# Performance work log

Measured on AMD Instinct MI355X. Metric: run time of the kernel, lower is better.

Reference implementation:

```python
import jax, jax.numpy as jnp
import numpy as np
from functools import partial
from jax import lax

THRESHOLD = 1.0
BETA = 4.0

@partial(jax.custom_vjp, nondiff_argnums=(1, 2))
def spike_fn(membrane, threshold, beta):
    # hard threshold forward
    return (membrane >= threshold).astype(membrane.dtype)

def _spike_fwd(membrane, threshold, beta):
    return spike_fn(membrane, threshold, beta), membrane

def _spike_bwd(threshold, beta, membrane, g):
    # fast-sigmoid surrogate gradient: 1 / (1 + beta*|u - theta|)^2
    x = membrane - threshold
    surrogate = 1.0 / (1.0 + beta * jnp.abs(x)) ** 2
    return (g * surrogate,)

spike_fn.defvjp(_spike_fwd, _spike_bwd)


def setup_inputs() -> dict:
    key = jax.random.key(0)
    k1, = jax.random.split(key, 1)
    x = jax.random.normal(k1, (64, 100, 4096), dtype=jnp.float32)
    # log_alpha = log(exp(-1/tau_mem)) = -1/tau_mem, tau_mem = 20.0
    log_alpha = jnp.asarray(-1.0 / 20.0, dtype=jnp.float32)
    return {"x": x, "log_alpha": log_alpha}


def reference(x, log_alpha):
    # x: (batch, time, features)
    alpha = jax.nn.sigmoid(log_alpha)  # membrane decay in (0,1)

    def step(u, xt):
        u = alpha * u + xt                    # leaky integration
        s = spike_fn(u, THRESHOLD, BETA)      # fire
        u = u - s * THRESHOLD                 # subtract-reset
        return u, s

    x_t = jnp.swapaxes(x, 0, 1)               # (T, B, F)
    u0 = jnp.zeros_like(x_t[0])
    _, spikes_t = lax.scan(step, u0, x_t)
    spikes = jnp.swapaxes(spikes_t, 0, 1)      # (B, T, F)
    rate = spikes.mean()
    return spikes, rate
```

## Files before the change

### kernel.cpp

```cpp
#include <hip/hip_runtime.h>
#include <math.h>


typedef float f32x2 __attribute__((ext_vector_type(2)));

constexpr int T_STEPS = 100;
constexpr int F2      = 2048;
constexpr int BATCH   = 64;
constexpr long long TOTAL = (long long)BATCH * T_STEPS * 4096;

__global__ __launch_bounds__(256)
void lif_fwd(const f32x2* __restrict__ x,
             const float* __restrict__ log_alpha,
             f32x2*       __restrict__ out,
             unsigned int* __restrict__ cnt) {
    int idx  = blockIdx.x * 256 + threadIdx.x;
    int b    = idx >> 11;
    int f2   = idx & 2047;
    size_t base = (size_t)b * T_STEPS * F2 + f2;

    double la = (double)log_alpha[0];
    float alpha = (float)(1.0 / (1.0 + exp(-la)));

    f32x2 u = {0.f, 0.f};
    unsigned int c = 0;

    #pragma unroll 10
    for (int t = 0; t < T_STEPS; ++t) {
        f32x2 xt = x[base + (size_t)t * F2];
        f32x2 s;
        float ux = __fadd_rn(__fmul_rn(alpha, u.x), xt.x);
        float uy = __fadd_rn(__fmul_rn(alpha, u.y), xt.y);
        s.x = (ux >= 1.0f) ? 1.0f : 0.0f;
        s.y = (uy >= 1.0f) ? 1.0f : 0.0f;
        u.x = ux - s.x;
        u.y = uy - s.y;
        __builtin_nontemporal_store(s, &out[base + (size_t)t * F2]);
        c += (unsigned)(s.x + s.y);
    }

    for (int off = 32; off > 0; off >>= 1)
        c += __shfl_down(c, off, 64);

    __shared__ unsigned int wsum[4];
    int lane = threadIdx.x & 63;
    int wid  = threadIdx.x >> 6;
    if (lane == 0) wsum[wid] = c;
    __syncthreads();
    if (threadIdx.x == 0) {
        unsigned int s = wsum[0] + wsum[1] + wsum[2] + wsum[3];
        atomicAdd(cnt, s);
    }
}

__global__ void lif_rate(const unsigned int* __restrict__ cnt,
                         float* __restrict__ rate_out) {
    rate_out[0] = (float)((double)cnt[0] / (double)TOTAL);
}

extern "C" void kernel_launch(void* const* d_in, const int* in_sizes, int n_in,
                              void* d_out, int out_size, void* d_ws, size_t ws_size,
                              hipStream_t stream) {
    const float* x  = (const float*)d_in[0];
    const float* la = (const float*)d_in[1];
    float* out = (float*)d_out;
    unsigned int* cnt = (unsigned int*)d_ws;

    (void)hipMemsetAsync(cnt, 0, sizeof(unsigned int), stream);

    int threads = BATCH * F2;
    lif_fwd<<<threads / 256, 256, 0, stream>>>(
        (const f32x2*)x, la, (f32x2*)out, cnt);

    lif_rate<<<1, 1, 0, stream>>>(cnt, out + TOTAL);
}
```

Baseline: 43.20 us.

## Use one feature per thread and replace atomic counter with per-block partial sums

Result: faster. 37.73 us, median of 2 (-12.7%).

```diff
diff --git a/kernel.cpp b/kernel.cpp
--- a/kernel.cpp
+++ b/kernel.cpp
@@ -2,41 +2,36 @@
 #include <math.h>
 
 
-typedef float f32x2 __attribute__((ext_vector_type(2)));
-
 constexpr int T_STEPS = 100;
-constexpr int F2      = 2048;
+constexpr int F       = 4096;
 constexpr int BATCH   = 64;
-constexpr long long TOTAL = (long long)BATCH * T_STEPS * 4096;
+constexpr int NBLOCKS = BATCH * F / 256;
+constexpr long long TOTAL = (long long)BATCH * T_STEPS * F;
 
 __global__ __launch_bounds__(256)
-void lif_fwd(const f32x2* __restrict__ x,
+void lif_fwd(const float* __restrict__ x,
              const float* __restrict__ log_alpha,
-             f32x2*       __restrict__ out,
-             unsigned int* __restrict__ cnt) {
+             float*       __restrict__ out,
+             unsigned int* __restrict__ blk_cnt) {
     int idx  = blockIdx.x * 256 + threadIdx.x;
-    int b    = idx >> 11;
-    int f2   = idx & 2047;
-    size_t base = (size_t)b * T_STEPS * F2 + f2;
+    int b    = idx >> 12;
+    int f    = idx & 4095;
+    size_t base = (size_t)b * T_STEPS * F + f;
 
     double la = (double)log_alpha[0];
     float alpha = (float)(1.0 / (1.0 + exp(-la)));
 
-    f32x2 u = {0.f, 0.f};
+    float u = 0.f;
     unsigned int c = 0;
 
     #pragma unroll 10
     for (int t = 0; t < T_STEPS; ++t) {
-        f32x2 xt = x[base + (size_t)t * F2];
-        f32x2 s;
-        float ux = __fadd_rn(__fmul_rn(alpha, u.x), xt.x);
-        float uy = __fadd_rn(__fmul_rn(alpha, u.y), xt.y);
-        s.x = (ux >= 1.0f) ? 1.0f : 0.0f;
-        s.y = (uy >= 1.0f) ? 1.0f : 0.0f;
-        u.x = ux - s.x;
-        u.y = uy - s.y;
-        __builtin_nontemporal_store(s, &out[base + (size_t)t * F2]);
-        c += (unsigned)(s.x + s.y);
+        float xt = x[base + (size_t)t * F];
+        u = __fadd_rn(__fmul_rn(alpha, u), xt);
+        float s = (u >= 1.0f) ? 1.0f : 0.0f;
+        u -= s;
+        __builtin_nontemporal_store(s, &out[base + (size_t)t * F]);
+        c += (unsigned)s;
     }
 
     for (int off = 32; off > 0; off >>= 1)
@@ -47,15 +42,28 @@
     int wid  = threadIdx.x >> 6;
     if (lane == 0) wsum[wid] = c;
     __syncthreads();
+    if (threadIdx.x == 0)
+        blk_cnt[blockIdx.x] = wsum[0] + wsum[1] + wsum[2] + wsum[3];
+}
+
+__global__ __launch_bounds__(256)
+void lif_rate(const unsigned int* __restrict__ blk_cnt,
+              float* __restrict__ rate_out) {
+    unsigned int c = 0;
+    #pragma unroll
+    for (int i = 0; i < NBLOCKS / 256; ++i)
+        c += blk_cnt[threadIdx.x + i * 256];
+    for (int off = 32; off > 0; off >>= 1)
+        c += __shfl_down(c, off, 64);
+    __shared__ unsigned int wsum[4];
+    int lane = threadIdx.x & 63;
+    int wid  = threadIdx.x >> 6;
+    if (lane == 0) wsum[wid] = c;
+    __syncthreads();
     if (threadIdx.x == 0) {
         unsigned int s = wsum[0] + wsum[1] + wsum[2] + wsum[3];
-        atomicAdd(cnt, s);
+        rate_out[0] = (float)((double)s / (double)TOTAL);
     }
-}
-
-__global__ void lif_rate(const unsigned int* __restrict__ cnt,
-                         float* __restrict__ rate_out) {
-    rate_out[0] = (float)((double)cnt[0] / (double)TOTAL);
 }
 
 extern "C" void kernel_launch(void* const* d_in, const int* in_sizes, int n_in,
@@ -64,13 +72,8 @@
     const float* x  = (const float*)d_in[0];
     const float* la = (const float*)d_in[1];
     float* out = (float*)d_out;
-    unsigned int* cnt = (unsigned int*)d_ws;
+    unsigned int* blk_cnt = (unsigned int*)d_ws;
 
-    (void)hipMemsetAsync(cnt, 0, sizeof(unsigned int), stream);
-
-    int threads = BATCH * F2;
-    lif_fwd<<<threads / 256, 256, 0, stream>>>(
-        (const f32x2*)x, la, (f32x2*)out, cnt);
-
-    lif_rate<<<1, 1, 0, stream>>>(cnt, out + TOTAL);
+    lif_fwd<<<NBLOCKS, 256, 0, stream>>>(x, la, out, blk_cnt);
+    lif_rate<<<1, 256, 0, stream>>>(blk_cnt, out + TOTAL);
 }
```
